# Kernel optimization log

Measured on AMD Instinct MI355X. Metric: run time of the kernel, lower is better.

Reference implementation:

```python
import jax, jax.numpy as jnp
import numpy as np

N_NODES = 50000
N_EDGES = 800000
D_IN = 128
D_HID = 128
N_CLS = 40


def setup_inputs() -> dict:
    key = jax.random.key(0)
    ks = jax.random.split(key, 9)
    x = jax.random.normal(ks[0], (N_NODES, D_IN), dtype=jnp.float32)
    edge_index = jax.random.randint(ks[1], (2, N_EDGES), 0, N_NODES, dtype=jnp.int64)
    def lin(k, fan_in, fan_out):
        bound = 1.0 / np.sqrt(fan_in)
        return jax.random.uniform(k, (fan_in, fan_out), jnp.float32, -bound, bound)
    params = {
        'w1_l': lin(ks[2], D_IN, D_HID), 'w1_r': lin(ks[3], D_IN, D_HID),
        'b1': jnp.zeros((D_HID,), jnp.float32),
        'w2_l': lin(ks[4], D_HID, D_HID), 'w2_r': lin(ks[5], D_HID, D_HID),
        'b2': jnp.zeros((D_HID,), jnp.float32),
        'w3_l': lin(ks[6], D_HID, N_CLS), 'w3_r': lin(ks[7], D_HID, N_CLS),
        'b3': jnp.zeros((N_CLS,), jnp.float32),
    }
    return {'x': x, 'edge_index': edge_index, **params}


def _sage_layer(x, src, dst, w_l, w_r, b):
    # mean-aggregate messages from src -> dst, then lin_l(agg) + lin_r(x) + b, relu
    msgs = x[src]                                             # [E, d] gather
    agg = jax.ops.segment_sum(msgs, dst, num_segments=x.shape[0])  # [N, d]
    deg = jax.ops.segment_sum(jnp.ones((src.shape[0],), x.dtype), dst,
                              num_segments=x.shape[0])        # [N]
    agg = agg / jnp.maximum(deg, 1.0)[:, None]
    out = agg @ w_l + x @ w_r + b
    return jax.nn.relu(out)  # dropout p=0.0 -> identity


def reference(x, edge_index, w1_l, w1_r, b1, w2_l, w2_r, b2, w3_l, w3_r, b3):
    src, dst = edge_index[0], edge_index[1]
    h = _sage_layer(x, src, dst, w1_l, w1_r, b1)
    h = _sage_layer(h, src, dst, w2_l, w2_r, b2)
    h = _sage_layer(h, src, dst, w3_l, w3_r, b3)
    return h
```

## Files before the change

### kernel.cpp

```cpp
#include <hip/hip_runtime.h>
#include <hip/hip_bf16.h>

#define NN 50000
#define NE 800000
#define DD 128
#define NCLS 40
#define NBK ((NN + 255) >> 8)
#define EPB 1024
#define PB ((NE + EPB - 1) / EPB)
#define CVB ((NN * DD / 4) / 256)
#define WB 384
#define SEMAX 5120
#define PR (NN + 1)
#define DCAP 48

typedef _Float16 f16x8 __attribute__((ext_vector_type(8)));
typedef _Float16 f16x4 __attribute__((ext_vector_type(4)));
typedef float f32x4 __attribute__((ext_vector_type(4)));

__device__ __forceinline__ unsigned int pack2h(_Float16 a, _Float16 b) {
    union { _Float16 h[2]; unsigned int u; } c;
    c.h[0] = a; c.h[1] = b;
    return c.u;
}
__device__ __forceinline__ void unpack2h(unsigned int p, float& a, float& b) {
    union { unsigned int u; _Float16 h[2]; } c;
    c.u = p;
    a = (float)c.h[0]; b = (float)c.h[1];
}


__global__ void k_front(const int* __restrict__ ei, int* __restrict__ cellcnt,
                        int* __restrict__ celloff, unsigned int* __restrict__ pairs,
                        const float* __restrict__ x, unsigned short* __restrict__ xh,
                        const float* __restrict__ w1l, const float* __restrict__ w1r,
                        const float* __restrict__ w2l, const float* __restrict__ w2r,
                        const float* __restrict__ w3l, const float* __restrict__ w3r,
                        unsigned short* __restrict__ bt1h,
                        unsigned short* __restrict__ bt2h,
                        unsigned short* __restrict__ bt3h,
                        unsigned short* __restrict__ h1h) {
    if (blockIdx.x >= PB + CVB) {
        int idx = blockIdx.x - (PB + CVB);
        if (idx == WB) {
            int t = threadIdx.x;
            if (t < 128) {
                int which = t >> 4;
                unsigned int* buf = (unsigned int*)((which < 4) ? xh : h1h);
                int plane = which & 3;
                buf[((size_t)plane * PR + NN) * 16 + (t & 15)] = 0u;
            }
            return;
        }
        int w = idx >> 1, half = idx & 1;
        int ks = w & 7, tmp = w >> 3;
        int nt = tmp & 7, layer = tmp >> 3;
        const int NT = (layer == 2) ? 3 : 8;
        const int NC = (layer == 2) ? NCLS : DD;
        if (nt >= NT) return;
        const float* wl = (layer == 0) ? w1l : (layer == 1) ? w2l : w3l;
        const float* wr = (layer == 0) ? w1r : (layer == 1) ? w2r : w3r;
        unsigned short* bh = (layer == 0) ? bt1h : (layer == 1) ? bt2h : bt3h;
        int t = threadIdx.x;
        int j = t & 7, lane = (t >> 3) + half * 32;
        int row = nt * 16 + (lane & 15);
        int k = ks * 32 + (lane >> 4) * 8 + j;
        float v = 0.f;
        if (row < NC)
            v = (k < 128) ? wl[(size_t)k * NC + row] : wr[(size_t)(k - 128) * NC + row];
        union { _Float16 f; unsigned short u; } ch;
        ch.f = (_Float16)v;
        bh[((size_t)(ks * NT + nt) * 64 + lane) * 8 + j] = ch.u;
        return;
    }
    if (blockIdx.x >= PB) {
        int i = (blockIdx.x - PB) * 256 + threadIdx.x;
        float4 v = ((const float4*)x)[i];
        f16x4 h;
        h[0] = (_Float16)v.x; h[1] = (_Float16)v.y;
        h[2] = (_Float16)v.z; h[3] = (_Float16)v.w;
        int row = i >> 5;
        int f = i & 31;
        int plane = f >> 3;
        int pc = (f & 7) * 4;
        *(f16x4*)(xh + ((size_t)plane * PR + row) * 32 + pc) = h;
        return;
    }
    __shared__ int hist[NBK];
    __shared__ int s[256];
    __shared__ unsigned int sE[EPB];
    __shared__ int nz;
    const int t = threadIdx.x, blk = blockIdx.x;
    const int e0 = blk * EPB;
    if (t == 0) nz = 0;
    for (int i = t; i < NBK; i += 256) hist[i] = 0;
    __syncthreads();
    int any = 0;
    for (int i = t; i < EPB; i += 256)
        if (ei[2 * e0 + 2 * i + 1] != 0) any = 1;
    if (any) atomicOr(&nz, 1);
    __syncthreads();
    const int is64 = (nz == 0);
    unsigned int v[EPB / 256];
    int eb[EPB / 256], er[EPB / 256];
#pragma unroll
    for (int j = 0; j < EPB / 256; ++j) {
        int e = e0 + j * 256 + t;
        if (e < NE) {
            int sv, d;
            if (is64) { sv = ei[2 * e]; d = ei[2 * (NE + e)]; }
            else      { sv = ei[e];     d = ei[NE + e]; }
            v[j] = ((unsigned)sv << 16) | (unsigned)d;
            eb[j] = d >> 8;
            er[j] = atomicAdd(&hist[eb[j]], 1);
        } else {
            eb[j] = -1;
        }
    }
    __syncthreads();
    int hv = (t < NBK) ? hist[t] : 0;
    s[t] = hv;
    __syncthreads();
#pragma unroll
    for (int off = 1; off < 256; off <<= 1) {
        int u = (t >= off) ? s[t - off] : 0;
        __syncthreads();
        s[t] += u;
        __syncthreads();
    }
#pragma unroll
    for (int j = 0; j < EPB / 256; ++j)
        if (eb[j] >= 0) sE[s[eb[j]] - hist[eb[j]] + er[j]] = v[j];
    __syncthreads();
    ((uint4*)(pairs + (size_t)blk * EPB))[t] = ((const uint4*)sE)[t];
    for (int i = t; i < NBK; i += 256) {
        cellcnt[(size_t)i * PB + blk] = hist[i];
        celloff[(size_t)i * PB + blk] = s[i] - hist[i];
    }
}

__global__ void k_scan_ba(const int* __restrict__ cellcnt, int* __restrict__ bsum) {
    __shared__ int red[256];
    int b = blockIdx.x, t = threadIdx.x;
    int acc = 0;
    for (int i = t; i < PB; i += 256) acc += cellcnt[(size_t)b * PB + i];
    red[t] = acc;
    __syncthreads();
#pragma unroll
    for (int off = 128; off > 0; off >>= 1) {
        if (t < off) red[t] += red[t + off];
        __syncthreads();
    }
    if (t == 0) bsum[b] = red[0];
}

__global__ void k_fill2(const unsigned int* __restrict__ pairs,
                        const int* __restrict__ cellcnt,
                        const int* __restrict__ celloff,
                        const int* __restrict__ bsum,
                        int* __restrict__ row_ptr, unsigned short* __restrict__ srcs) {
    __shared__ unsigned int sE[SEMAX];
    __shared__ int hist[256];
    __shared__ int cur[256];
    __shared__ int sb[256];
    __shared__ int scnt;
    const int b = blockIdx.x, t = threadIdx.x;
    if (t < 256) {
        int v = (t < NBK) ? bsum[t] : 0;
        sb[t] = v;
    }
    if (t == 0) scnt = 0;
    if (t < 256) hist[t] = 0;
    __syncthreads();
#pragma unroll
    for (int off = 1; off < 256; off <<= 1) {
        int u = (t >= off && t < 256) ? sb[t - off] : 0;
        __syncthreads();
        if (t < 256) sb[t] += u;
        __syncthreads();
    }
    const int bbase = (b == 0) ? 0 : sb[b - 1];
    if (b == NBK - 1 && t == 0) row_ptr[NN] = sb[NBK - 1];
    for (int blk = t; blk < PB; blk += 512) {
        int cnt = cellcnt[(size_t)b * PB + blk];
        if (cnt) {
            int off = celloff[(size_t)b * PB + blk];
            int base = atomicAdd(&scnt, cnt);
            if (base + cnt <= SEMAX) {
                const unsigned int* pp = pairs + (size_t)blk * EPB + off;
                for (int j = 0; j < cnt; ++j) {
                    unsigned int v = pp[j];
                    sE[base + j] = v;
                    atomicAdd(&hist[v & 255u], 1);
                }
            }
        }
    }
    __syncthreads();
    int h = (t < 256) ? hist[t] : 0;
    if (t < 256) cur[t] = h;
    __syncthreads();
#pragma unroll
    for (int off = 1; off < 256; off <<= 1) {
        int u = (t >= off && t < 256) ? cur[t - off] : 0;
        __syncthreads();
        if (t < 256) cur[t] += u;
        __syncthreads();
    }
    if (t < 256) {
        int node = (b << 8) + t;
        int base = bbase + cur[t] - h;
        if (node < NN) row_ptr[node] = base;
        cur[t] = base;
    }
    __syncthreads();
    int total = min(scnt, SEMAX);
    for (int i = t; i < total; i += 512) {
        unsigned int v = sE[i];
        int pos = atomicAdd(&cur[v & 255u], 1);
        srcs[pos] = (unsigned short)(v >> 16);
    }
}

__global__ __launch_bounds__(256, 8)
void k_aggp(const unsigned int* __restrict__ inq, const int* __restrict__ row_ptr,
            const unsigned short* __restrict__ srcs, unsigned int* __restrict__ oq) {
    __shared__ unsigned short sSrc[16 * DCAP];
    __shared__ int sRp[17];
    const int t = threadIdx.x;
    const int plane = (blockIdx.x & 7) >> 1;
    const int c = ((blockIdx.x >> 3) << 1) + (blockIdx.x & 1);
    if (c >= NN / 16) return;
    const int n0 = c * 16;
    if (t < 17) sRp[t] = row_ptr[n0 + t];
    __syncthreads();
    {
        int ln = t >> 4, k2 = t & 15;
        int b = sRp[ln], e = sRp[ln + 1];
#pragma unroll
        for (int m = 0; m < DCAP / 16; ++m) {
            int k = k2 + m * 16;
            sSrc[ln * DCAP + k] = (b + k < e) ? srcs[b + k] : (unsigned short)NN;
        }
    }
    __syncthreads();
    const int wave = t >> 6, lane = t & 63;
    const int ng = lane >> 4;
    const unsigned int pc = lane & 15;
    const int ln = (wave << 2) + ng;
    const unsigned int* __restrict__ tab = inq + (size_t)plane * (PR * 16);
    const int b = sRp[ln], e = sRp[ln + 1];
    const int deg = e - b;
    int dm = deg;
    dm = max(dm, __shfl_xor(dm, 16));
    dm = max(dm, __shfl_xor(dm, 32));
    const int capped = min(dm, DCAP);
    const int nit = (capped + 3) >> 2;
    float a0 = 0.f, a1 = 0.f;
    int sb = ln * DCAP;
    for (int it = 0; it < nit; ++it) {
        unsigned int s0 = sSrc[sb + 0];
        unsigned int s1 = sSrc[sb + 1];
        unsigned int s2 = sSrc[sb + 2];
        unsigned int s3 = sSrc[sb + 3];
        unsigned int p0 = tab[s0 * 16u + pc];
        unsigned int p1 = tab[s1 * 16u + pc];
        unsigned int p2 = tab[s2 * 16u + pc];
        unsigned int p3 = tab[s3 * 16u + pc];
        float u0, u1;
        unpack2h(p0, u0, u1); a0 += u0; a1 += u1;
        unpack2h(p1, u0, u1); a0 += u0; a1 += u1;
        unpack2h(p2, u0, u1); a0 += u0; a1 += u1;
        unpack2h(p3, u0, u1); a0 += u0; a1 += u1;
        sb += 4;
    }
    if (dm > DCAP) {
        for (int k = DCAP; k < deg; ++k) {
            unsigned int s = (unsigned int)srcs[b + k];
            unsigned int p = tab[s * 16u + pc];
            float u0, u1;
            unpack2h(p, u0, u1);
            a0 += u0; a1 += u1;
        }
    }
    float inv = 1.0f / (float)(deg > 0 ? deg : 1);
    unsigned int ov = pack2h((_Float16)(a0 * inv), (_Float16)(a1 * inv));
    __builtin_nontemporal_store(ov, &oq[((size_t)plane * PR + (n0 + ln)) * 16 + pc]);
}

template <int NT, int KPS, bool PACKOUT>
__launch_bounds__(256, 4)
__global__ void k_mfma(const unsigned short* __restrict__ A1h,
                       const unsigned short* __restrict__ A2h,
                       const unsigned short* __restrict__ Bthf,
                       const float* __restrict__ bias, float* __restrict__ outf,
                       unsigned short* __restrict__ outh, const int NC) {
    constexpr int STAGE_ELEMS = KPS * NT * 64 * 8;
    constexpr int STAGE_U4 = STAGE_ELEMS / 8;
    __shared__ unsigned short sBh[STAGE_ELEMS];

    const int tid = threadIdx.x;
    const int wave = tid >> 6, lane = tid & 63;
    const int quad = lane >> 4, mr = lane & 15;
    const int m0 = blockIdx.x * 64 + wave * 16;
    const int row = m0 + mr;
    const bool rok = row < NN;

    f32x4 acc[NT] = {};
    const f16x8 zero = {};

    auto aload = [&](int ks) -> f16x8 {
        const unsigned short* base = (ks < 4) ? A1h : A2h;
        const int plane = ks & 3;
        return rok ? *(const f16x8*)(base + ((size_t)plane * PR + row) * 32 + quad * 8)
                   : zero;
    };

    f16x8 cah = aload(0), pah;

#pragma unroll
    for (int s = 0; s < 8 / KPS; ++s) {
        const uint4* gh = (const uint4*)(Bthf + (size_t)s * STAGE_ELEMS);
        uint4* lh = (uint4*)sBh;
        if (s) __syncthreads();
        for (int i = tid; i < STAGE_U4; i += 256) lh[i] = gh[i];
        __syncthreads();

#pragma unroll
        for (int kl = 0; kl < KPS; ++kl) {
            const int ks = s * KPS + kl;
            if (ks < 7) pah = aload(ks + 1);
#pragma unroll
            for (int n = 0; n < NT; ++n) {
                const int fo = ((kl * NT + n) * 64 + lane) * 8;
                f16x8 bh = *(const f16x8*)(sBh + fo);
                acc[n] = __builtin_amdgcn_mfma_f32_16x16x32_f16(cah, bh, acc[n], 0, 0, 0);
            }
            cah = pah;
        }
    }

#pragma unroll
    for (int n = 0; n < NT; ++n) {
        int col = n * 16 + mr;
        float bv = (col < NC) ? bias[col] : 0.f;
#pragma unroll
        for (int r = 0; r < 4; ++r) {
            int orow = m0 + quad * 4 + r;
            if (orow < NN && col < NC) {
                float v = acc[n][r] + bv;
                v = v > 0.f ? v : 0.f;
                if (PACKOUT) {
                    union { _Float16 f; unsigned short u; } ch;
                    ch.f = (_Float16)v;
                    int pl = col >> 5, pcc = col & 31;
                    outh[((size_t)pl * PR + orow) * 32 + pcc] = ch.u;
                } else {
                    outf[(size_t)orow * NC + col] = v;
                }
            }
        }
    }
}

__global__ __launch_bounds__(256, 4)
void k_gemm3(const unsigned short* __restrict__ Ah,
             const unsigned short* __restrict__ Bthf,
             const float* __restrict__ bias,
             unsigned short* __restrict__ zh, float* __restrict__ yf) {
    __shared__ unsigned short sBh[8 * 3 * 64 * 8];
    const int tid = threadIdx.x;
    const int wave = tid >> 6, lane = tid & 63;
    const int quad = lane >> 4, mr = lane & 15;
    const int m0 = blockIdx.x * 64 + wave * 16;
    const int row = m0 + mr;
    const bool rok = row < NN;

    const uint4* gh = (const uint4*)Bthf;
    uint4* lh = (uint4*)sBh;
    for (int i = tid; i < (8 * 3 * 64 * 8) / 8; i += 256) lh[i] = gh[i];

    const f16x8 zero = {};
    f16x8 a[4];
#pragma unroll
    for (int j = 0; j < 4; ++j)
        a[j] = rok ? *(const f16x8*)(Ah + ((size_t)j * PR + row) * 32 + quad * 8)
                   : zero;
    __syncthreads();

    f32x4 accl[3] = {}, accr[3] = {};
#pragma unroll
    for (int ks = 0; ks < 4; ++ks) {
#pragma unroll
        for (int n = 0; n < 3; ++n) {
            f16x8 bl = *(const f16x8*)(sBh + ((ks * 3 + n) * 64 + lane) * 8);
            accl[n] = __builtin_amdgcn_mfma_f32_16x16x32_f16(a[ks], bl, accl[n], 0, 0, 0);
            f16x8 br = *(const f16x8*)(sBh + (((ks + 4) * 3 + n) * 64 + lane) * 8);
            accr[n] = __builtin_amdgcn_mfma_f32_16x16x32_f16(a[ks], br, accr[n], 0, 0, 0);
        }
    }

#pragma unroll
    for (int n = 0; n < 3; ++n) {
        int col = n * 16 + mr;
        float bv = (col < NCLS) ? bias[col] : 0.f;
#pragma unroll
        for (int r = 0; r < 4; ++r) {
            int orow = m0 + quad * 4 + r;
            if (orow < NN) {
                union { _Float16 f; unsigned short u; } ch;
                ch.f = (_Float16)accl[n][r];
                zh[(size_t)orow * 64 + col] = ch.u;
                if (col < NCLS) yf[(size_t)orow * 40 + col] = accr[n][r] + bv;
            }
        }
    }
}

template <int J>
__device__ __forceinline__ void acc3(const uint2* __restrict__ tab,
                                     const unsigned short* __restrict__ srcs,
                                     int i, int eg, int cg, float* a) {
    uint2 p[J];
#pragma unroll
    for (int j = 0; j < J; ++j)
        p[j] = tab[(size_t)srcs[i + j * 4 + eg] * 16 + cg];
#pragma unroll
    for (int j = 0; j < J; ++j) {
        float u0, u1;
        unpack2h(p[j].x, u0, u1); a[0] += u0; a[1] += u1;
        unpack2h(p[j].y, u0, u1); a[2] += u0; a[3] += u1;
    }
}

__global__ __launch_bounds__(256, 8)
void k_agg3(const unsigned int* __restrict__ zu,
            const int* __restrict__ row_ptr,
            const unsigned short* __restrict__ srcs,
            const float* __restrict__ yf, float* __restrict__ out) {
    const int node = blockIdx.x * 4 + (threadIdx.x >> 6);
    const int lane = threadIdx.x & 63;
    const int eg = lane >> 4, cg = lane & 15;
    const uint2* tab = (const uint2*)zu;
    const int b = row_ptr[node], e = row_ptr[node + 1];
    const int deg = e - b;
    float a[4] = {};
    int i = b;
    while (i + 16 <= e) { acc3<4>(tab, srcs, i, eg, cg, a); i += 16; }
    if (i + 8 <= e) { acc3<2>(tab, srcs, i, eg, cg, a); i += 8; }
    if (i + 4 <= e) { acc3<1>(tab, srcs, i, eg, cg, a); i += 4; }
    int rem = e - i;
    if (rem > 0) {
        int idx = i + eg;
        if (idx > e - 1) idx = e - 1;
        uint2 p = tab[(size_t)srcs[idx] * 16 + cg];
        if (eg < rem) {
            float u0, u1;
            unpack2h(p.x, u0, u1); a[0] += u0; a[1] += u1;
            unpack2h(p.y, u0, u1); a[2] += u0; a[3] += u1;
        }
    }
#pragma unroll
    for (int k = 0; k < 4; ++k) {
        a[k] += __shfl_xor(a[k], 16);
        a[k] += __shfl_xor(a[k], 32);
    }
    if (eg == 0 && cg < 10) {
        float inv = 1.0f / (float)(deg > 0 ? deg : 1);
        float4 yv = ((const float4*)yf)[(size_t)node * 10 + cg];
        float4 o;
        o.x = fmaxf(a[0] * inv + yv.x, 0.f);
        o.y = fmaxf(a[1] * inv + yv.y, 0.f);
        o.z = fmaxf(a[2] * inv + yv.z, 0.f);
        o.w = fmaxf(a[3] * inv + yv.w, 0.f);
        ((float4*)out)[(size_t)node * 10 + cg] = o;
    }
}

extern "C" void kernel_launch(void* const* d_in, const int* in_sizes, int n_in,
                              void* d_out, int out_size, void* d_ws, size_t ws_size,
                              hipStream_t stream) {
    const float* x    = (const float*)d_in[0];
    const int*   ei   = (const int*)d_in[1];
    const float* w1_l = (const float*)d_in[2];
    const float* w1_r = (const float*)d_in[3];
    const float* b1   = (const float*)d_in[4];
    const float* w2_l = (const float*)d_in[5];
    const float* w2_r = (const float*)d_in[6];
    const float* b2   = (const float*)d_in[7];
    const float* w3_l = (const float*)d_in[8];
    const float* w3_r = (const float*)d_in[9];
    const float* b3   = (const float*)d_in[10];
    float* out = (float*)d_out;

    char* w = (char*)d_ws;
    size_t off = 0;
    auto alloc = [&](size_t bytes) -> void* {
        void* p = w + off;
        off += (bytes + 255) / 256 * 256;
        return p;
    };
    int* row_ptr = (int*)alloc((size_t)(NN + 1) * 4);
    unsigned short* srcs = (unsigned short*)alloc((size_t)NE * 2 + 64);
    int* cellcnt = (int*)alloc((size_t)NBK * PB * 4);
    int* celloff = (int*)alloc((size_t)NBK * PB * 4);
    int* bsum    = (int*)alloc((size_t)NBK * 4);
    unsigned int* pairs = (unsigned int*)alloc((size_t)PB * EPB * 4);
    unsigned short* xh   = (unsigned short*)alloc((size_t)4 * PR * 32 * 2);
    unsigned short* aggh = (unsigned short*)alloc((size_t)4 * PR * 32 * 2);
    unsigned short* h1h  = (unsigned short*)alloc((size_t)4 * PR * 32 * 2);
    unsigned short* zh   = (unsigned short*)alloc((size_t)NN * 64 * 2);
    float*          yf   = (float*)alloc((size_t)NN * 40 * 4);
    unsigned short* bt1h = (unsigned short*)alloc((size_t)8 * 8 * 64 * 8 * 2);
    unsigned short* bt2h = (unsigned short*)alloc((size_t)8 * 8 * 64 * 8 * 2);
    unsigned short* bt3h = (unsigned short*)alloc((size_t)8 * 3 * 64 * 8 * 2);
    unsigned short* h2h = xh;
    (void)ws_size;

    k_front<<<PB + CVB + WB + 1, 256, 0, stream>>>(ei, cellcnt, celloff, pairs, x, xh,
                                                   w1_l, w1_r, w2_l, w2_r, w3_l, w3_r,
                                                   bt1h, bt2h, bt3h, h1h);
    k_scan_ba<<<NBK, 256, 0, stream>>>(cellcnt, bsum);
    k_fill2<<<NBK, 512, 0, stream>>>(pairs, cellcnt, celloff, bsum, row_ptr, srcs);

    const int gmb = (NN + 63) / 64;
    const int gp  = 8 * ((NN / 16 + 1) / 2);
    k_aggp<<<gp, 256, 0, stream>>>((const unsigned int*)xh, row_ptr, srcs,
                                   (unsigned int*)aggh);
    k_mfma<8, 4, true><<<gmb, 256, 0, stream>>>(aggh, xh, bt1h, b1,
                                                nullptr, h1h, DD);
    k_aggp<<<gp, 256, 0, stream>>>((const unsigned int*)h1h, row_ptr, srcs,
                                   (unsigned int*)aggh);
    k_mfma<8, 4, true><<<gmb, 256, 0, stream>>>(aggh, h1h, bt2h, b2,
                                                nullptr, h2h, DD);
    k_gemm3<<<gmb, 256, 0, stream>>>(h2h, bt3h, b3, zh, yf);
    k_agg3<<<NN / 4, 256, 0, stream>>>((const unsigned int*)zh, row_ptr, srcs,
                                       yf, out);
}
```

Baseline: 227.3 us.

## Widen per-lane gathers in aggregation kernels and stage 32 nodes per block

k_aggp now has each block handle 32 nodes with 8 lanes per node, and each lane loads a uint2 (4 halves) instead of one packed pair. k_agg3 is rewritten to the same shared-memory source-staging scheme, with uint4 gathers and 8 nodes per wave in place of one node per wave with a shuffle reduction. A zeroed pad row is added to zh so padded source indices read zeros. The aim is fewer, wider gather instructions and less reduction overhead, at the cost of more registers per lane and fewer threads in flight per node.

New measurement: 221.7 us. -2.5%, faster.

```diff
diff --git a/kernel.cpp b/kernel.cpp
--- a/kernel.cpp
+++ b/kernel.cpp
@@ -13,6 +13,7 @@
 #define SEMAX 5120
 #define PR (NN + 1)
 #define DCAP 48
+#define NCH ((NN + 31) / 32)
 
 typedef _Float16 f16x8 __attribute__((ext_vector_type(8)));
 typedef _Float16 f16x4 __attribute__((ext_vector_type(4)));
@@ -39,7 +40,8 @@
                         unsigned short* __restrict__ bt1h,
                         unsigned short* __restrict__ bt2h,
                         unsigned short* __restrict__ bt3h,
-                        unsigned short* __restrict__ h1h) {
+                        unsigned short* __restrict__ h1h,
+                        unsigned short* __restrict__ zh) {
     if (blockIdx.x >= PB + CVB) {
         int idx = blockIdx.x - (PB + CVB);
         if (idx == WB) {
@@ -49,6 +51,8 @@
                 unsigned int* buf = (unsigned int*)((which < 4) ? xh : h1h);
                 int plane = which & 3;
                 buf[((size_t)plane * PR + NN) * 16 + (t & 15)] = 0u;
+            } else if (t < 160) {
+                ((unsigned int*)zh)[(size_t)NN * 32 + (t - 128)] = 0u;
             }
             return;
         }
@@ -225,67 +229,78 @@
 __global__ __launch_bounds__(256, 8)
 void k_aggp(const unsigned int* __restrict__ inq, const int* __restrict__ row_ptr,
             const unsigned short* __restrict__ srcs, unsigned int* __restrict__ oq) {
-    __shared__ unsigned short sSrc[16 * DCAP];
-    __shared__ int sRp[17];
+    __shared__ unsigned short sSrc[32 * DCAP];
+    __shared__ int sRp[33];
     const int t = threadIdx.x;
     const int plane = (blockIdx.x & 7) >> 1;
     const int c = ((blockIdx.x >> 3) << 1) + (blockIdx.x & 1);
-    if (c >= NN / 16) return;
-    const int n0 = c * 16;
-    if (t < 17) sRp[t] = row_ptr[n0 + t];
+    if (c >= NCH) return;
+    const int n0 = c * 32;
+    if (t < 33) sRp[t] = row_ptr[min(n0 + t, NN)];
     __syncthreads();
     {
-        int ln = t >> 4, k2 = t & 15;
+        int ln = t >> 3, k2 = t & 7;
         int b = sRp[ln], e = sRp[ln + 1];
 #pragma unroll
-        for (int m = 0; m < DCAP / 16; ++m) {
-            int k = k2 + m * 16;
+        for (int m = 0; m < DCAP / 8; ++m) {
+            int k = k2 + m * 8;
             sSrc[ln * DCAP + k] = (b + k < e) ? srcs[b + k] : (unsigned short)NN;
         }
     }
     __syncthreads();
     const int wave = t >> 6, lane = t & 63;
-    const int ng = lane >> 4;
-    const unsigned int pc = lane & 15;
-    const int ln = (wave << 2) + ng;
-    const unsigned int* __restrict__ tab = inq + (size_t)plane * (PR * 16);
+    const int ng = lane >> 3;
+    const unsigned int pc = lane & 7;
+    const int ln = (wave << 3) + ng;
+    const uint2* __restrict__ tab = (const uint2*)inq + (size_t)plane * (PR * 8);
     const int b = sRp[ln], e = sRp[ln + 1];
     const int deg = e - b;
     int dm = deg;
+    dm = max(dm, __shfl_xor(dm, 8));
     dm = max(dm, __shfl_xor(dm, 16));
     dm = max(dm, __shfl_xor(dm, 32));
-    const int capped = min(dm, DCAP);
-    const int nit = (capped + 3) >> 2;
-    float a0 = 0.f, a1 = 0.f;
+    const int nit = (min(dm, DCAP) + 3) >> 2;
+    float a0 = 0.f, a1 = 0.f, a2 = 0.f, a3 = 0.f;
     int sb = ln * DCAP;
     for (int it = 0; it < nit; ++it) {
         unsigned int s0 = sSrc[sb + 0];
         unsigned int s1 = sSrc[sb + 1];
         unsigned int s2 = sSrc[sb + 2];
         unsigned int s3 = sSrc[sb + 3];
-        unsigned int p0 = tab[s0 * 16u + pc];
-        unsigned int p1 = tab[s1 * 16u + pc];
-        unsigned int p2 = tab[s2 * 16u + pc];
-        unsigned int p3 = tab[s3 * 16u + pc];
+        uint2 p0 = tab[s0 * 8u + pc];
+        uint2 p1 = tab[s1 * 8u + pc];
+        uint2 p2 = tab[s2 * 8u + pc];
+        uint2 p3 = tab[s3 * 8u + pc];
         float u0, u1;
-        unpack2h(p0, u0, u1); a0 += u0; a1 += u1;
-        unpack2h(p1, u0, u1); a0 += u0; a1 += u1;
-        unpack2h(p2, u0, u1); a0 += u0; a1 += u1;
-        unpack2h(p3, u0, u1); a0 += u0; a1 += u1;
+        unpack2h(p0.x, u0, u1); a0 += u0; a1 += u1;
+        unpack2h(p0.y, u0, u1); a2 += u0; a3 += u1;
+        unpack2h(p1.x, u0, u1); a0 += u0; a1 += u1;
+        unpack2h(p1.y, u0, u1); a2 += u0; a3 += u1;
+        unpack2h(p2.x, u0, u1); a0 += u0; a1 += u1;
+        unpack2h(p2.y, u0, u1); a2 += u0; a3 += u1;
+        unpack2h(p3.x, u0, u1); a0 += u0; a1 += u1;
+        unpack2h(p3.y, u0, u1); a2 += u0; a3 += u1;
         sb += 4;
     }
     if (dm > DCAP) {
         for (int k = DCAP; k < deg; ++k) {
             unsigned int s = (unsigned int)srcs[b + k];
-            unsigned int p = tab[s * 16u + pc];
+            uint2 p = tab[s * 8u + pc];
             float u0, u1;
-            unpack2h(p, u0, u1);
-            a0 += u0; a1 += u1;
-        }
-    }
-    float inv = 1.0f / (float)(deg > 0 ? deg : 1);
-    unsigned int ov = pack2h((_Float16)(a0 * inv), (_Float16)(a1 * inv));
-    __builtin_nontemporal_store(ov, &oq[((size_t)plane * PR + (n0 + ln)) * 16 + pc]);
+            unpack2h(p.x, u0, u1); a0 += u0; a1 += u1;
+            unpack2h(p.y, u0, u1); a2 += u0; a3 += u1;
+        }
+    }
+    const int node = n0 + ln;
+    if (node < NN) {
+        float inv = 1.0f / (float)(deg > 0 ? deg : 1);
+        union { uint2 v2; unsigned long long u64; } ov;
+        ov.v2.x = pack2h((_Float16)(a0 * inv), (_Float16)(a1 * inv));
+        ov.v2.y = pack2h((_Float16)(a2 * inv), (_Float16)(a3 * inv));
+        unsigned long long* dst =
+            (unsigned long long*)(oq + ((size_t)plane * PR + node) * 16) + pc;
+        __builtin_nontemporal_store(ov.u64, dst);
+    }
 }
 
 template <int NT, int KPS, bool PACKOUT>
@@ -417,63 +432,97 @@
     }
 }
 
-template <int J>
-__device__ __forceinline__ void acc3(const uint2* __restrict__ tab,
-                                     const unsigned short* __restrict__ srcs,
-                                     int i, int eg, int cg, float* a) {
-    uint2 p[J];
-#pragma unroll
-    for (int j = 0; j < J; ++j)
-        p[j] = tab[(size_t)srcs[i + j * 4 + eg] * 16 + cg];
-#pragma unroll
-    for (int j = 0; j < J; ++j) {
-        float u0, u1;
-        unpack2h(p[j].x, u0, u1); a[0] += u0; a[1] += u1;
-        unpack2h(p[j].y, u0, u1); a[2] += u0; a[3] += u1;
-    }
-}
-
 __global__ __launch_bounds__(256, 8)
 void k_agg3(const unsigned int* __restrict__ zu,
             const int* __restrict__ row_ptr,
             const unsigned short* __restrict__ srcs,
             const float* __restrict__ yf, float* __restrict__ out) {
-    const int node = blockIdx.x * 4 + (threadIdx.x >> 6);
-    const int lane = threadIdx.x & 63;
-    const int eg = lane >> 4, cg = lane & 15;
-    const uint2* tab = (const uint2*)zu;
-    const int b = row_ptr[node], e = row_ptr[node + 1];
+    __shared__ unsigned short sSrc[32 * DCAP];
+    __shared__ int sRp[33];
+    const int t = threadIdx.x;
+    const int c = blockIdx.x;
+    const int n0 = c * 32;
+    if (t < 33) sRp[t] = row_ptr[min(n0 + t, NN)];
+    __syncthreads();
+    {
+        int ln = t >> 3, k2 = t & 7;
+        int b = sRp[ln], e = sRp[ln + 1];
+#pragma unroll
+        for (int m = 0; m < DCAP / 8; ++m) {
+            int k = k2 + m * 8;
+            sSrc[ln * DCAP + k] = (b + k < e) ? srcs[b + k] : (unsigned short)NN;
+        }
+    }
+    __syncthreads();
+    const int wave = t >> 6, lane = t & 63;
+    const int ng = lane >> 3;
+    const unsigned int pc = lane & 7;
+    const int ln = (wave << 3) + ng;
+    const uint4* __restrict__ tab = (const uint4*)zu;
+    const int b = sRp[ln], e = sRp[ln + 1];
     const int deg = e - b;
-    float a[4] = {};
-    int i = b;
-    while (i + 16 <= e) { acc3<4>(tab, srcs, i, eg, cg, a); i += 16; }
-    if (i + 8 <= e) { acc3<2>(tab, srcs, i, eg, cg, a); i += 8; }
-    if (i + 4 <= e) { acc3<1>(tab, srcs, i, eg, cg, a); i += 4; }
-    int rem = e - i;
-    if (rem > 0) {
-        int idx = i + eg;
-        if (idx > e - 1) idx = e - 1;
-        uint2 p = tab[(size_t)srcs[idx] * 16 + cg];
-        if (eg < rem) {
+    int dm = deg;
+    dm = max(dm, __shfl_xor(dm, 8));
+    dm = max(dm, __shfl_xor(dm, 16));
+    dm = max(dm, __shfl_xor(dm, 32));
+    const int nit = (min(dm, DCAP) + 3) >> 2;
+    float a[8] = {};
+    int sb = ln * DCAP;
+    for (int it = 0; it < nit; ++it) {
+        unsigned int s0 = sSrc[sb + 0];
+        unsigned int s1 = sSrc[sb + 1];
+        unsigned int s2 = sSrc[sb + 2];
+        unsigned int s3 = sSrc[sb + 3];
+        uint4 p0 = tab[s0 * 8u + pc];
+        uint4 p1 = tab[s1 * 8u + pc];
+        uint4 p2 = tab[s2 * 8u + pc];
+        uint4 p3 = tab[s3 * 8u + pc];
+        float u0, u1;
+        unpack2h(p0.x, u0, u1); a[0] += u0; a[1] += u1;
+        unpack2h(p0.y, u0, u1); a[2] += u0; a[3] += u1;
+        unpack2h(p0.z, u0, u1); a[4] += u0; a[5] += u1;
+        unpack2h(p0.w, u0, u1); a[6] += u0; a[7] += u1;
+        unpack2h(p1.x, u0, u1); a[0] += u0; a[1] += u1;
+        unpack2h(p1.y, u0, u1); a[2] += u0; a[3] += u1;
+        unpack2h(p1.z, u0, u1); a[4] += u0; a[5] += u1;
+        unpack2h(p1.w, u0, u1); a[6] += u0; a[7] += u1;
+        unpack2h(p2.x, u0, u1); a[0] += u0; a[1] += u1;
+        unpack2h(p2.y, u0, u1); a[2] += u0; a[3] += u1;
+        unpack2h(p2.z, u0, u1); a[4] += u0; a[5] += u1;
+        unpack2h(p2.w, u0, u1); a[6] += u0; a[7] += u1;
+        unpack2h(p3.x, u0, u1); a[0] += u0; a[1] += u1;
+        unpack2h(p3.y, u0, u1); a[2] += u0; a[3] += u1;
+        unpack2h(p3.z, u0, u1); a[4] += u0; a[5] += u1;
+        unpack2h(p3.w, u0, u1); a[6] += u0; a[7] += u1;
+        sb += 4;
+    }
+    if (dm > DCAP) {
+        for (int k = DCAP; k < deg; ++k) {
+            unsigned int s = (unsigned int)srcs[b + k];
+            uint4 p = tab[s * 8u + pc];
             float u0, u1;
             unpack2h(p.x, u0, u1); a[0] += u0; a[1] += u1;
             unpack2h(p.y, u0, u1); a[2] += u0; a[3] += u1;
-        }
-    }
-#pragma unroll
-    for (int k = 0; k < 4; ++k) {
-        a[k] += __shfl_xor(a[k], 16);
-        a[k] += __shfl_xor(a[k], 32);
-    }
-    if (eg == 0 && cg < 10) {
+            unpack2h(p.z, u0, u1); a[4] += u0; a[5] += u1;
+            unpack2h(p.w, u0, u1); a[6] += u0; a[7] += u1;
+        }
+    }
+    const int node = n0 + ln;
+    if (node < NN && pc < 5) {
         float inv = 1.0f / (float)(deg > 0 ? deg : 1);
-        float4 yv = ((const float4*)yf)[(size_t)node * 10 + cg];
-        float4 o;
-        o.x = fmaxf(a[0] * inv + yv.x, 0.f);
-        o.y = fmaxf(a[1] * inv + yv.y, 0.f);
-        o.z = fmaxf(a[2] * inv + yv.z, 0.f);
-        o.w = fmaxf(a[3] * inv + yv.w, 0.f);
-        ((float4*)out)[(size_t)node * 10 + cg] = o;
+        float4 y0 = ((const float4*)yf)[(size_t)node * 10 + pc * 2];
+        float4 y1 = ((const float4*)yf)[(size_t)node * 10 + pc * 2 + 1];
+        float4 o0, o1;
+        o0.x = fmaxf(a[0] * inv + y0.x, 0.f);
+        o0.y = fmaxf(a[1] * inv + y0.y, 0.f);
+        o0.z = fmaxf(a[2] * inv + y0.z, 0.f);
+        o0.w = fmaxf(a[3] * inv + y0.w, 0.f);
+        o1.x = fmaxf(a[4] * inv + y1.x, 0.f);
+        o1.y = fmaxf(a[5] * inv + y1.y, 0.f);
+        o1.z = fmaxf(a[6] * inv + y1.z, 0.f);
+        o1.w = fmaxf(a[7] * inv + y1.w, 0.f);
+        ((float4*)out)[(size_t)node * 10 + pc * 2] = o0;
+        ((float4*)out)[(size_t)node * 10 + pc * 2 + 1] = o1;
     }
 }
 
@@ -509,7 +558,7 @@
     unsigned short* xh   = (unsigned short*)alloc((size_t)4 * PR * 32 * 2);
     unsigned short* aggh = (unsigned short*)alloc((size_t)4 * PR * 32 * 2);
     unsigned short* h1h  = (unsigned short*)alloc((size_t)4 * PR * 32 * 2);
-    unsigned short* zh   = (unsigned short*)alloc((size_t)NN * 64 * 2);
+    unsigned short* zh   = (unsigned short*)alloc((size_t)PR * 64 * 2);
     float*          yf   = (float*)alloc((size_t)NN * 40 * 4);
     unsigned short* bt1h = (unsigned short*)alloc((size_t)8 * 8 * 64 * 8 * 2);
     unsigned short* bt2h = (unsigned short*)alloc((size_t)8 * 8 * 64 * 8 * 2);
@@ -519,12 +568,12 @@
 
     k_front<<<PB + CVB + WB + 1, 256, 0, stream>>>(ei, cellcnt, celloff, pairs, x, xh,
                                                    w1_l, w1_r, w2_l, w2_r, w3_l, w3_r,
-                                                   bt1h, bt2h, bt3h, h1h);
+                                                   bt1h, bt2h, bt3h, h1h, zh);
     k_scan_ba<<<NBK, 256, 0, stream>>>(cellcnt, bsum);
     k_fill2<<<NBK, 512, 0, stream>>>(pairs, cellcnt, celloff, bsum, row_ptr, srcs);
 
     const int gmb = (NN + 63) / 64;
-    const int gp  = 8 * ((NN / 16 + 1) / 2);
+    const int gp  = 8 * ((NCH + 1) / 2);
     k_aggp<<<gp, 256, 0, stream>>>((const unsigned int*)xh, row_ptr, srcs,
                                    (unsigned int*)aggh);
     k_mfma<8, 4, true><<<gmb, 256, 0, stream>>>(aggh, xh, bt1h, b1,
@@ -534,6 +583,6 @@
     k_mfma<8, 4, true><<<gmb, 256, 0, stream>>>(aggh, h1h, bt2h, b2,
                                                 nullptr, h2h, DD);
     k_gemm3<<<gmb, 256, 0, stream>>>(h2h, bt3h, b3, zh, yf);
-    k_agg3<<<NN / 4, 256, 0, stream>>>((const unsigned int*)zh, row_ptr, srcs,
-                                       yf, out);
-}
+    k_agg3<<<NCH, 256, 0, stream>>>((const unsigned int*)zh, row_ptr, srcs,
+                                    yf, out);
+}
```
